# Optimization experiments

Measured on AMD Instinct MI355X. Metric: run time of the kernel, lower is better.

The kernel has to match this reference:

```python
import jax, jax.numpy as jnp
import numpy as np

D_MODEL = 1024
N_HEADS = 16
B, T = 2, 2048


def setup_inputs() -> dict:
    key = jax.random.key(0)
    ks = jax.random.split(key, 5)
    scale = 1.0 / np.sqrt(D_MODEL)
    return {
        "x": jax.random.normal(ks[0], (B, T, D_MODEL), dtype=jnp.float32),
        "W_q": jax.random.normal(ks[1], (D_MODEL, D_MODEL), dtype=jnp.float32) * scale,
        "W_k": jax.random.normal(ks[2], (D_MODEL, D_MODEL), dtype=jnp.float32) * scale,
        "W_v": jax.random.normal(ks[3], (D_MODEL, D_MODEL), dtype=jnp.float32) * scale,
        "W_o": jax.random.normal(ks[4], (D_MODEL, D_MODEL), dtype=jnp.float32) * scale,
    }


def reference(x, W_q, W_k, W_v, W_o):
    Bn, Tn, D = x.shape
    H = N_HEADS
    Dh = D // H
    # nn.Linear(x) = x @ W.T ; weights stored as [out, in]
    q = (x @ W_q.T).reshape(Bn, Tn, H, Dh).transpose(0, 2, 1, 3)  # [B,H,T,Dh]
    k = (x @ W_k.T).reshape(Bn, Tn, H, Dh).transpose(0, 2, 1, 3)
    v = (x @ W_v.T).reshape(Bn, Tn, H, Dh).transpose(0, 2, 1, 3)
    scores = jnp.einsum("bhqd,bhkd->bhqk", q, k) / np.sqrt(Dh).astype(np.float32)
    attn = jax.nn.softmax(scores, axis=-1)  # [B,H,T,T]
    out = jnp.einsum("bhqk,bhkd->bhqd", attn, v)  # [B,H,T,Dh]
    out = out.transpose(0, 2, 1, 3).reshape(Bn, Tn, D)
    return out @ W_o.T
```

## Files before the change

### kernel.cpp

```cpp
#include <hip/hip_runtime.h>
#include <stdint.h>
#include <stddef.h>


typedef __bf16  bf16x8  __attribute__((ext_vector_type(8)));
typedef __bf16  bf16x4  __attribute__((ext_vector_type(4)));
typedef float   floatx4 __attribute__((ext_vector_type(4)));
typedef short   short4v __attribute__((ext_vector_type(4)));

#define DEV static __device__ __forceinline__

DEV void ld_g2l16(const void* g, void* l) {
    __builtin_amdgcn_global_load_lds(
        (__attribute__((address_space(1))) void*)g,
        (__attribute__((address_space(3))) void*)l,
        16, 0, 0);
}

DEV floatx4 mfma16(bf16x4 a, bf16x4 b, floatx4 c) {
#if defined(__HIP_DEVICE_COMPILE__)
    return __builtin_amdgcn_mfma_f32_16x16x16bf16_1k(
        __builtin_bit_cast(short4v, a), __builtin_bit_cast(short4v, b),
        c, 0, 0, 0);
#else
    (void)a; (void)b;
    return c;
#endif
}

#define WK_SCALE 0.18033688011112042f

__global__ __launch_bounds__(256) void cvt_all(
    const float* __restrict__ x,
    const float* __restrict__ wq, const float* __restrict__ wk,
    const float* __restrict__ wv, const float* __restrict__ wo,
    __bf16* __restrict__ xb,
    __bf16* __restrict__ wqb, __bf16* __restrict__ wkb,
    __bf16* __restrict__ wvb, __bf16* __restrict__ wob)
{
    unsigned u = blockIdx.x * 256u + threadIdx.x;
    const float* src;
    __bf16* dst;
    unsigned off;
    float mul = 1.0f;
    if (u < 1048576u) {
        src = x; dst = xb; off = u;
    } else {
        unsigned u2 = u - 1048576u;
        unsigned sel = u2 >> 18;
        off = u2 & 0x3FFFFu;
        src = (sel == 0) ? wq : (sel == 1) ? wk : (sel == 2) ? wv : wo;
        dst = (sel == 0) ? wqb : (sel == 1) ? wkb : (sel == 2) ? wvb : wob;
        if (sel == 1) mul = WK_SCALE;
    }
    float4 f = *(const float4*)(src + (size_t)off * 4);
    bf16x4 o = { (__bf16)(f.x * mul), (__bf16)(f.y * mul),
                 (__bf16)(f.z * mul), (__bf16)(f.w * mul) };
    *(bf16x4*)(dst + (size_t)off * 4) = o;
}

template<int BM, int NMAT, bool OUT_F32, bool TR_V>
__global__ __launch_bounds__(256) void gemm_bt(
    const __bf16* __restrict__ A,
    const __bf16* __restrict__ B0, const __bf16* __restrict__ B1,
    const __bf16* __restrict__ B2,
    void* __restrict__ C0, void* __restrict__ C1, void* __restrict__ C2)
{
    constexpr int Kd = 1024;
    constexpr int N  = 1024;
    constexpr int MI = BM / 32;
    constexpr int NA = BM / 64;
    __shared__ __bf16 As[BM * 32];
    __shared__ __bf16 Bs[128 * 32];

    const int t    = threadIdx.x;
    const int wid  = __builtin_amdgcn_readfirstlane(t >> 6);
    const int lane = t & 63;
    const int quad = lane >> 4;
    const int l15  = lane & 15;

    const int bx  = blockIdx.x;
    const int mat = (NMAT > 1) ? (bx >> 3) : 0;
    const int bn  = (NMAT > 1) ? (bx & 7)  : bx;
    const int bm  = blockIdx.y;
    const __bf16* Bm = (mat == 0) ? B0 : (mat == 1) ? B1 : B2;

    const __bf16* pA[NA];
    const __bf16* pB[2];
#pragma unroll
    for (int i = 0; i < NA; ++i) {
        int c    = i * 256 + t;
        int row  = c >> 2;
        int g    = (c & 3) ^ ((row >> 1) & 3);
        pA[i] = A + (size_t)(bm * BM + row) * Kd + g * 8;
    }
#pragma unroll
    for (int i = 0; i < 2; ++i) {
        int c    = i * 256 + t;
        int row  = c >> 2;
        int g    = (c & 3) ^ ((row >> 1) & 3);
        pB[i] = Bm + (size_t)(bn * 128 + row) * Kd + g * 8;
    }

    const int wm = wid >> 1;
    const int wn = wid & 1;
    const int slotr = quad ^ ((l15 >> 1) & 3);

    floatx4 acc[MI][4];
    const floatx4 z = { 0.f, 0.f, 0.f, 0.f };
#pragma unroll
    for (int i = 0; i < MI; ++i)
#pragma unroll
        for (int j = 0; j < 4; ++j) acc[i][j] = z;

    for (int kb = 0; kb < Kd; kb += 32) {
        __syncthreads();
#pragma unroll
        for (int i = 0; i < NA; ++i)
            ld_g2l16(pA[i] + kb, (char*)As + i * 4096 + wid * 1024);
#pragma unroll
        for (int i = 0; i < 2; ++i)
            ld_g2l16(pB[i] + kb, (char*)Bs + i * 4096 + wid * 1024);
        __syncthreads();

        bf16x8 af[MI], bf[4];
#pragma unroll
        for (int i = 0; i < MI; ++i) {
            int rowA = wm * (BM / 2) + i * 16 + l15;
            af[i] = *(const bf16x8*)&As[rowA * 32 + slotr * 8];
        }
#pragma unroll
        for (int j = 0; j < 4; ++j) {
            int rowB = wn * 64 + j * 16 + l15;
            bf[j] = *(const bf16x8*)&Bs[rowB * 32 + slotr * 8];
        }
#pragma unroll
        for (int i = 0; i < MI; ++i)
#pragma unroll
            for (int j = 0; j < 4; ++j)
                acc[i][j] = __builtin_amdgcn_mfma_f32_16x16x32_bf16(
                    af[i], bf[j], acc[i][j], 0, 0, 0);
    }

    const int row0 = bm * BM + wm * (BM / 2);
    const int col0 = bn * 128 + wn * 64;

    if (TR_V && mat == 2) {
        __bf16* Vt = (__bf16*)C2;
        const int bq    = bm >> 4;
        const int tloc0 = (row0 & 2047) + quad * 4;
#pragma unroll
        for (int i = 0; i < MI; ++i)
#pragma unroll
            for (int j = 0; j < 4; ++j) {
                int col = col0 + j * 16 + l15;
                int hh  = col >> 6, dh = col & 63;
                bf16x4 v = { (__bf16)acc[i][j][0], (__bf16)acc[i][j][1],
                             (__bf16)acc[i][j][2], (__bf16)acc[i][j][3] };
                *(bf16x4*)(Vt + ((size_t)(bq * 16 + hh) * 64 + dh) * 2048
                              + tloc0 + i * 16) = v;
            }
    } else {
        void* Cv = (mat == 0) ? C0 : (mat == 1) ? C1 : C2;
#pragma unroll
        for (int i = 0; i < MI; ++i)
#pragma unroll
            for (int j = 0; j < 4; ++j)
#pragma unroll
                for (int r = 0; r < 4; ++r) {
                    int grow = row0 + i * 16 + quad * 4 + r;
                    int gcol = col0 + j * 16 + l15;
                    if (OUT_F32)
                        ((float*)Cv)[(size_t)grow * N + gcol] = acc[i][j][r];
                    else
                        ((__bf16*)Cv)[(size_t)grow * N + gcol] =
                            (__bf16)acc[i][j][r];
                }
    }
}

__global__ __launch_bounds__(256, 2) void flash_kernel(
    const __bf16* __restrict__ Q, const __bf16* __restrict__ K,
    const __bf16* __restrict__ Vt, __bf16* __restrict__ O)
{
    __shared__ __bf16 Qs[128 * 64];
    __shared__ __bf16 Ks[2][64 * 64];
    __shared__ __bf16 Vs[2][64 * 64];

    const int t    = threadIdx.x;
    const int wid  = __builtin_amdgcn_readfirstlane(t >> 6);
    const int half = wid >> 1;
    const int wsub = wid & 1;
    const int lane = t & 63;
    const int quad = lane >> 4;
    const int l15  = lane & 15;
    const int qt   = blockIdx.x;
    const int bh   = blockIdx.y;
    const int b    = bh >> 4, h = bh & 15;

#pragma unroll
    for (int i = 0; i < 4; ++i) {
        int c = i * 256 + t;
        int row = c >> 3;
        int g   = (c & 7) ^ (row & 7);
        ld_g2l16(Q + (size_t)(b * 2048 + qt * 128 + row) * 1024 + h * 64 + g * 8,
                 (char*)Qs + i * 4096 + wid * 1024);
    }

    const __bf16* pK[2];
    const __bf16* pV[2];
#pragma unroll
    for (int i = 0; i < 2; ++i) {
        int c = i * 256 + t;
        int srow = c >> 3;
        int sg   = (c & 7) ^ (srow & 7);
        pK[i] = K  + (size_t)(b * 2048 + srow) * 1024 + h * 64 + sg * 8;
        pV[i] = Vt + (size_t)(bh * 64 + srow) * 2048 + sg * 8;
    }

    __syncthreads();

    bf16x8 qf[4][2];
#pragma unroll
    for (int nb = 0; nb < 4; ++nb)
#pragma unroll
        for (int ks = 0; ks < 2; ++ks) {
            int row  = wsub * 64 + nb * 16 + l15;
            int slot = (ks * 4 + quad) ^ (row & 7);
            qf[nb][ks] = *(const bf16x8*)&Qs[row * 64 + slot * 8];
        }

    int koff[2];
#pragma unroll
    for (int ks = 0; ks < 2; ++ks)
        koff[ks] = l15 * 128 + (((ks * 4 + quad) ^ (l15 & 7)) << 4);
    int voff[4];
#pragma unroll
    for (int k16 = 0; k16 < 4; ++k16)
        voff[k16] = l15 * 128 + (((k16 * 2 + (quad >> 1)) ^ (l15 & 7)) << 4)
                  + (quad & 1) * 8;

    const floatx4 z = { 0.f, 0.f, 0.f, 0.f };
    floatx4 o[4][4];
#pragma unroll
    for (int nb = 0; nb < 4; ++nb)
#pragma unroll
        for (int nd = 0; nd < 4; ++nd) o[nb][nd] = z;
    float lsum[4] = { 0.f, 0.f, 0.f, 0.f };

    for (int it = 0; it < 16; ++it) {
        __syncthreads();
#pragma unroll
        for (int i = 0; i < 2; ++i) {
            ld_g2l16(pK[i] + (size_t)it * 65536,
                     (char*)Ks[0] + i * 4096 + wid * 1024);
            ld_g2l16(pK[i] + (size_t)(16 + it) * 65536,
                     (char*)Ks[1] + i * 4096 + wid * 1024);
            ld_g2l16(pV[i] + it * 64,
                     (char*)Vs[0] + i * 4096 + wid * 1024);
            ld_g2l16(pV[i] + (16 + it) * 64,
                     (char*)Vs[1] + i * 4096 + wid * 1024);
        }
        __syncthreads();

        const char* kbase = (const char*)Ks[half];
        const char* vbase = (const char*)Vs[half];
#pragma unroll
        for (int kt16 = 0; kt16 < 4; ++kt16) {
            floatx4 s[4] = { z, z, z, z };
#pragma unroll
            for (int ks = 0; ks < 2; ++ks) {
                bf16x8 kf = *(const bf16x8*)(kbase + kt16 * 2048 + koff[ks]);
#pragma unroll
                for (int nb = 0; nb < 4; ++nb)
                    s[nb] = __builtin_amdgcn_mfma_f32_16x16x32_bf16(
                        kf, qf[nb][ks], s[nb], 0, 0, 0);
            }
            bf16x4 pb[4];
#pragma unroll
            for (int nb = 0; nb < 4; ++nb) {
                float p0 = __builtin_amdgcn_exp2f(s[nb][0]);
                float p1 = __builtin_amdgcn_exp2f(s[nb][1]);
                float p2 = __builtin_amdgcn_exp2f(s[nb][2]);
                float p3 = __builtin_amdgcn_exp2f(s[nb][3]);
                lsum[nb] += (p0 + p1) + (p2 + p3);
                bf16x4 pw = { (__bf16)p0, (__bf16)p1, (__bf16)p2, (__bf16)p3 };
                pb[nb] = pw;
            }
#pragma unroll
            for (int nd = 0; nd < 4; ++nd) {
                bf16x4 va = *(const bf16x4*)(vbase + nd * 2048 + voff[kt16]);
#pragma unroll
                for (int nb = 0; nb < 4; ++nb)
                    o[nb][nd] = mfma16(va, pb[nb], o[nb][nd]);
            }
        }
    }

    __syncthreads();
    float* obuf = (wsub == 0) ? (float*)&Ks[0][0] : (float*)&Vs[0][0];
    float* lbuf = (float*)&Qs[0] + wsub * 256;
    if (half == 1) {
#pragma unroll
        for (int nb = 0; nb < 4; ++nb)
#pragma unroll
            for (int nd = 0; nd < 4; ++nd)
                *(floatx4*)(obuf + (nb * 4 + nd) * 256 + lane * 4) = o[nb][nd];
#pragma unroll
        for (int nb = 0; nb < 4; ++nb) lbuf[nb * 64 + lane] = lsum[nb];
    }
    __syncthreads();
    if (half == 0) {
#pragma unroll
        for (int nb = 0; nb < 4; ++nb)
#pragma unroll
            for (int nd = 0; nd < 4; ++nd)
                o[nb][nd] += *(const floatx4*)(obuf + (nb * 4 + nd) * 256
                                               + lane * 4);
#pragma unroll
        for (int nb = 0; nb < 4; ++nb) {
            lsum[nb] += lbuf[nb * 64 + lane];
            lsum[nb] += __shfl_xor(lsum[nb], 16);
            lsum[nb] += __shfl_xor(lsum[nb], 32);
        }
#pragma unroll
        for (int nb = 0; nb < 4; ++nb) {
            float inv = 1.f / lsum[nb];
            int token = qt * 128 + wsub * 64 + nb * 16 + l15;
#pragma unroll
            for (int nd = 0; nd < 4; ++nd) {
                bf16x4 ov = { (__bf16)(o[nb][nd][0] * inv),
                              (__bf16)(o[nb][nd][1] * inv),
                              (__bf16)(o[nb][nd][2] * inv),
                              (__bf16)(o[nb][nd][3] * inv) };
                *(bf16x4*)(O + (size_t)(b * 2048 + token) * 1024
                             + h * 64 + nd * 16 + quad * 4) = ov;
            }
        }
    }
}

extern "C" void kernel_launch(void* const* d_in, const int* in_sizes, int n_in,
                              void* d_out, int out_size, void* d_ws, size_t ws_size,
                              hipStream_t stream)
{
    const float* x  = (const float*)d_in[0];
    const float* wq = (const float*)d_in[1];
    const float* wk = (const float*)d_in[2];
    const float* wv = (const float*)d_in[3];
    const float* wo = (const float*)d_in[4];

    char* ws = (char*)d_ws;
    __bf16* xb  = (__bf16*)(ws + 0);
    __bf16* wqb = (__bf16*)(ws + 8388608);
    __bf16* wkb = (__bf16*)(ws + 10485760);
    __bf16* wvb = (__bf16*)(ws + 12582912);
    __bf16* wob = (__bf16*)(ws + 14680064);
    __bf16* Qb  = (__bf16*)(ws + 16777216);
    __bf16* Kb  = (__bf16*)(ws + 25165824);
    __bf16* Vtb = (__bf16*)(ws + 33554432);
    __bf16* Ob  = xb;

    cvt_all<<<8192, 256, 0, stream>>>(x, wq, wk, wv, wo, xb, wqb, wkb, wvb, wob);

    gemm_bt<128, 3, false, true><<<dim3(24, 32), 256, 0, stream>>>(
        xb, wqb, wkb, wvb, (void*)Qb, (void*)Kb, (void*)Vtb);

    flash_kernel<<<dim3(16, 32), 256, 0, stream>>>(Qb, Kb, Vtb, Ob);

    gemm_bt<64, 1, true, false><<<dim3(8, 64), 256, 0, stream>>>(
        Ob, wob, nullptr, nullptr, d_out, nullptr, nullptr);
}
```

Measured before the change: 176.8 us.

## Double-buffer K/V tiles in flash attention and raise MFMA wave priority

The K and V shared-memory tiles become double-buffered. The next iteration's global-to-LDS loads are issued before the current tile is computed, so memory latency overlaps the MFMA work, and the two barriers per iteration drop to one. Each MFMA section is also wrapped in s_setprio so matrix work is favoured over the exp/convert section of other waves. This raises LDS use per block, which may limit occupancy at two blocks per CU.

New measurement: 185.5 us. 1.05x slower.

```diff
diff --git a/kernel.cpp b/kernel.cpp
--- a/kernel.cpp
+++ b/kernel.cpp
@@ -184,8 +184,8 @@
     const __bf16* __restrict__ Vt, __bf16* __restrict__ O)
 {
     __shared__ __bf16 Qs[128 * 64];
-    __shared__ __bf16 Ks[2][64 * 64];
-    __shared__ __bf16 Vs[2][64 * 64];
+    __shared__ __bf16 Ks[2][2][64 * 64];
+    __shared__ __bf16 Vs[2][2][64 * 64];
 
     const int t    = threadIdx.x;
     const int wid  = __builtin_amdgcn_readfirstlane(t >> 6);
@@ -218,6 +218,21 @@
         pV[i] = Vt + (size_t)(bh * 64 + srow) * 2048 + sg * 8;
     }
 
+    auto stage_kv = [&](int it2, int buf) {
+#pragma unroll
+        for (int i = 0; i < 2; ++i) {
+            ld_g2l16(pK[i] + (size_t)it2 * 65536,
+                     (char*)Ks[buf][0] + i * 4096 + wid * 1024);
+            ld_g2l16(pK[i] + (size_t)(16 + it2) * 65536,
+                     (char*)Ks[buf][1] + i * 4096 + wid * 1024);
+            ld_g2l16(pV[i] + it2 * 64,
+                     (char*)Vs[buf][0] + i * 4096 + wid * 1024);
+            ld_g2l16(pV[i] + (16 + it2) * 64,
+                     (char*)Vs[buf][1] + i * 4096 + wid * 1024);
+        }
+    };
+
+    stage_kv(0, 0);
     __syncthreads();
 
     bf16x8 qf[4][2];
@@ -248,26 +263,16 @@
         for (int nd = 0; nd < 4; ++nd) o[nb][nd] = z;
     float lsum[4] = { 0.f, 0.f, 0.f, 0.f };
 
+    int cur = 0;
     for (int it = 0; it < 16; ++it) {
-        __syncthreads();
-#pragma unroll
-        for (int i = 0; i < 2; ++i) {
-            ld_g2l16(pK[i] + (size_t)it * 65536,
-                     (char*)Ks[0] + i * 4096 + wid * 1024);
-            ld_g2l16(pK[i] + (size_t)(16 + it) * 65536,
-                     (char*)Ks[1] + i * 4096 + wid * 1024);
-            ld_g2l16(pV[i] + it * 64,
-                     (char*)Vs[0] + i * 4096 + wid * 1024);
-            ld_g2l16(pV[i] + (16 + it) * 64,
-                     (char*)Vs[1] + i * 4096 + wid * 1024);
-        }
-        __syncthreads();
-
-        const char* kbase = (const char*)Ks[half];
-        const char* vbase = (const char*)Vs[half];
+        if (it < 15) stage_kv(it + 1, cur ^ 1);
+
+        const char* kbase = (const char*)Ks[cur][half];
+        const char* vbase = (const char*)Vs[cur][half];
 #pragma unroll
         for (int kt16 = 0; kt16 < 4; ++kt16) {
             floatx4 s[4] = { z, z, z, z };
+            __builtin_amdgcn_s_setprio(1);
 #pragma unroll
             for (int ks = 0; ks < 2; ++ks) {
                 bf16x8 kf = *(const bf16x8*)(kbase + kt16 * 2048 + koff[ks]);
@@ -276,6 +281,7 @@
                     s[nb] = __builtin_amdgcn_mfma_f32_16x16x32_bf16(
                         kf, qf[nb][ks], s[nb], 0, 0, 0);
             }
+            __builtin_amdgcn_s_setprio(0);
             bf16x4 pb[4];
 #pragma unroll
             for (int nb = 0; nb < 4; ++nb) {
@@ -287,6 +293,7 @@
                 bf16x4 pw = { (__bf16)p0, (__bf16)p1, (__bf16)p2, (__bf16)p3 };
                 pb[nb] = pw;
             }
+            __builtin_amdgcn_s_setprio(1);
 #pragma unroll
             for (int nd = 0; nd < 4; ++nd) {
                 bf16x4 va = *(const bf16x4*)(vbase + nd * 2048 + voff[kt16]);
@@ -294,11 +301,14 @@
                 for (int nb = 0; nb < 4; ++nb)
                     o[nb][nd] = mfma16(va, pb[nb], o[nb][nd]);
             }
-        }
-    }
-
-    __syncthreads();
-    float* obuf = (wsub == 0) ? (float*)&Ks[0][0] : (float*)&Vs[0][0];
+            __builtin_amdgcn_s_setprio(0);
+        }
+        __syncthreads();
+        cur ^= 1;
+    }
+
+    float* obuf = (wsub == 0) ? (float*)&Ks[0][0][0]
+                              : (float*)&Vs[0][0][0];
     float* lbuf = (float*)&Qs[0] + wsub * 256;
     if (half == 1) {
 #pragma unroll
```

## Split flash attention key range four ways per block with smaller query tiles

Applied to the files above, without the earlier changes.

The flash kernel now handles 64 query rows per block instead of 128. Each of the four waves processes a different quarter of the key sequence, in 32-key chunks per iteration, and a multi-stage LDS reduction merges the partial outputs and row sums at the end. The grid doubles to 1024 blocks, launch bounds allow 4 blocks per CU, and block indices are swizzled so that blocks sharing a head are spread out. The aim is more parallelism and occupancy to better fill the GPU, at the cost of more reduction passes and barriers and more K/V reloading per query row.

After: 273.7 us. +54.9%, slower.

```diff
diff --git a/kernel.cpp b/kernel.cpp
--- a/kernel.cpp
+++ b/kernel.cpp
@@ -179,44 +179,40 @@
     }
 }
 
-__global__ __launch_bounds__(256, 2) void flash_kernel(
+__global__ __launch_bounds__(256, 4) void flash_kernel(
     const __bf16* __restrict__ Q, const __bf16* __restrict__ K,
     const __bf16* __restrict__ Vt, __bf16* __restrict__ O)
 {
-    __shared__ __bf16 Qs[128 * 64];
-    __shared__ __bf16 Ks[2][64 * 64];
-    __shared__ __bf16 Vs[2][64 * 64];
+    __shared__ __bf16 Qs[64 * 64];
+    __shared__ __bf16 Ks[4][32 * 64];
+    __shared__ __bf16 Vs[4][64 * 32];
 
     const int t    = threadIdx.x;
     const int wid  = __builtin_amdgcn_readfirstlane(t >> 6);
-    const int half = wid >> 1;
-    const int wsub = wid & 1;
     const int lane = t & 63;
     const int quad = lane >> 4;
     const int l15  = lane & 15;
-    const int qt   = blockIdx.x;
-    const int bh   = blockIdx.y;
+    const int flat = blockIdx.y * 32 + blockIdx.x;
+    const int swz  = (flat & 7) * 128 + (flat >> 3);
+    const int qt   = swz & 31;
+    const int bh   = swz >> 5;
     const int b    = bh >> 4, h = bh & 15;
 
 #pragma unroll
-    for (int i = 0; i < 4; ++i) {
+    for (int i = 0; i < 2; ++i) {
         int c = i * 256 + t;
         int row = c >> 3;
         int g   = (c & 7) ^ (row & 7);
-        ld_g2l16(Q + (size_t)(b * 2048 + qt * 128 + row) * 1024 + h * 64 + g * 8,
+        ld_g2l16(Q + (size_t)(b * 2048 + qt * 64 + row) * 1024 + h * 64 + g * 8,
                  (char*)Qs + i * 4096 + wid * 1024);
     }
 
-    const __bf16* pK[2];
-    const __bf16* pV[2];
-#pragma unroll
-    for (int i = 0; i < 2; ++i) {
-        int c = i * 256 + t;
-        int srow = c >> 3;
-        int sg   = (c & 7) ^ (srow & 7);
-        pK[i] = K  + (size_t)(b * 2048 + srow) * 1024 + h * 64 + sg * 8;
-        pV[i] = Vt + (size_t)(bh * 64 + srow) * 2048 + sg * 8;
-    }
+    const int srowK = t >> 3;
+    const int sgK   = (t & 7) ^ (srowK & 7);
+    const __bf16* pK0 = K + (size_t)(b * 2048 + srowK) * 1024 + h * 64 + sgK * 8;
+    const int srowV = t >> 2;
+    const int sgV   = (t & 3) ^ (srowV & 3);
+    const __bf16* pV0 = Vt + (size_t)(bh * 64 + srowV) * 2048 + sgV * 8;
 
     __syncthreads();
 
@@ -225,7 +221,7 @@
     for (int nb = 0; nb < 4; ++nb)
 #pragma unroll
         for (int ks = 0; ks < 2; ++ks) {
-            int row  = wsub * 64 + nb * 16 + l15;
+            int row  = nb * 16 + l15;
             int slot = (ks * 4 + quad) ^ (row & 7);
             qf[nb][ks] = *(const bf16x8*)&Qs[row * 64 + slot * 8];
         }
@@ -234,11 +230,11 @@
 #pragma unroll
     for (int ks = 0; ks < 2; ++ks)
         koff[ks] = l15 * 128 + (((ks * 4 + quad) ^ (l15 & 7)) << 4);
-    int voff[4];
-#pragma unroll
-    for (int k16 = 0; k16 < 4; ++k16)
-        voff[k16] = l15 * 128 + (((k16 * 2 + (quad >> 1)) ^ (l15 & 7)) << 4)
-                  + (quad & 1) * 8;
+    int voff[2];
+#pragma unroll
+    for (int kt = 0; kt < 2; ++kt)
+        voff[kt] = l15 * 64 + (((kt * 2 + (quad >> 1)) ^ (l15 & 3)) << 4)
+                 + (quad & 1) * 8;
 
     const floatx4 z = { 0.f, 0.f, 0.f, 0.f };
     floatx4 o[4][4];
@@ -251,26 +247,23 @@
     for (int it = 0; it < 16; ++it) {
         __syncthreads();
 #pragma unroll
-        for (int i = 0; i < 2; ++i) {
-            ld_g2l16(pK[i] + (size_t)it * 65536,
-                     (char*)Ks[0] + i * 4096 + wid * 1024);
-            ld_g2l16(pK[i] + (size_t)(16 + it) * 65536,
-                     (char*)Ks[1] + i * 4096 + wid * 1024);
-            ld_g2l16(pV[i] + it * 64,
-                     (char*)Vs[0] + i * 4096 + wid * 1024);
-            ld_g2l16(pV[i] + (16 + it) * 64,
-                     (char*)Vs[1] + i * 4096 + wid * 1024);
-        }
+        for (int tq = 0; tq < 4; ++tq)
+            ld_g2l16(pK0 + ((size_t)tq * 512 + it * 32) * 1024,
+                     (char*)Ks + tq * 4096 + wid * 1024);
+#pragma unroll
+        for (int tq = 0; tq < 4; ++tq)
+            ld_g2l16(pV0 + tq * 512 + it * 32,
+                     (char*)Vs + tq * 4096 + wid * 1024);
         __syncthreads();
 
-        const char* kbase = (const char*)Ks[half];
-        const char* vbase = (const char*)Vs[half];
-#pragma unroll
-        for (int kt16 = 0; kt16 < 4; ++kt16) {
+        const char* kbase = (const char*)Ks + wid * 4096;
+        const char* vbase = (const char*)Vs + wid * 4096;
+#pragma unroll
+        for (int kt = 0; kt < 2; ++kt) {
             floatx4 s[4] = { z, z, z, z };
 #pragma unroll
             for (int ks = 0; ks < 2; ++ks) {
-                bf16x8 kf = *(const bf16x8*)(kbase + kt16 * 2048 + koff[ks]);
+                bf16x8 kf = *(const bf16x8*)(kbase + kt * 2048 + koff[ks]);
 #pragma unroll
                 for (int nb = 0; nb < 4; ++nb)
                     s[nb] = __builtin_amdgcn_mfma_f32_16x16x32_bf16(
@@ -289,7 +282,7 @@
             }
 #pragma unroll
             for (int nd = 0; nd < 4; ++nd) {
-                bf16x4 va = *(const bf16x4*)(vbase + nd * 2048 + voff[kt16]);
+                bf16x4 va = *(const bf16x4*)(vbase + nd * 1024 + voff[kt]);
 #pragma unroll
                 for (int nb = 0; nb < 4; ++nb)
                     o[nb][nd] = mfma16(va, pb[nb], o[nb][nd]);
@@ -298,35 +291,71 @@
     }
 
     __syncthreads();
-    float* obuf = (wsub == 0) ? (float*)&Ks[0][0] : (float*)&Vs[0][0];
-    float* lbuf = (float*)&Qs[0] + wsub * 256;
-    if (half == 1) {
-#pragma unroll
-        for (int nb = 0; nb < 4; ++nb)
-#pragma unroll
-            for (int nd = 0; nd < 4; ++nd)
-                *(floatx4*)(obuf + (nb * 4 + nd) * 256 + lane * 4) = o[nb][nd];
-#pragma unroll
-        for (int nb = 0; nb < 4; ++nb) lbuf[nb * 64 + lane] = lsum[nb];
+    float* kb = (float*)&Ks[0][0];
+    float* vb = (float*)&Vs[0][0];
+    float* lb = (float*)&Qs[0];
+#pragma unroll
+    for (int nb = 0; nb < 4; ++nb)
+        lb[wid * 256 + nb * 64 + lane] = lsum[nb];
+    if (wid == 1) {
+#pragma unroll
+        for (int nb = 0; nb < 4; ++nb)
+#pragma unroll
+            for (int nd = 0; nd < 4; ++nd)
+                *(floatx4*)(kb + (nb * 4 + nd) * 256 + lane * 4) = o[nb][nd];
+    }
+    if (wid == 3) {
+#pragma unroll
+        for (int nb = 0; nb < 4; ++nb)
+#pragma unroll
+            for (int nd = 0; nd < 4; ++nd)
+                *(floatx4*)(vb + (nb * 4 + nd) * 256 + lane * 4) = o[nb][nd];
     }
     __syncthreads();
-    if (half == 0) {
-#pragma unroll
-        for (int nb = 0; nb < 4; ++nb)
-#pragma unroll
-            for (int nd = 0; nd < 4; ++nd)
-                o[nb][nd] += *(const floatx4*)(obuf + (nb * 4 + nd) * 256
+    if (wid == 0) {
+#pragma unroll
+        for (int nb = 0; nb < 4; ++nb)
+#pragma unroll
+            for (int nd = 0; nd < 4; ++nd)
+                o[nb][nd] += *(const floatx4*)(kb + (nb * 4 + nd) * 256
                                                + lane * 4);
+    }
+    if (wid == 2) {
+#pragma unroll
+        for (int nb = 0; nb < 4; ++nb)
+#pragma unroll
+            for (int nd = 0; nd < 4; ++nd)
+                o[nb][nd] += *(const floatx4*)(vb + (nb * 4 + nd) * 256
+                                               + lane * 4);
+    }
+    __syncthreads();
+    if (wid == 2) {
+#pragma unroll
+        for (int nb = 0; nb < 4; ++nb)
+#pragma unroll
+            for (int nd = 0; nd < 4; ++nd)
+                *(floatx4*)(kb + (nb * 4 + nd) * 256 + lane * 4) = o[nb][nd];
+    }
+    __syncthreads();
+    if (wid == 0) {
+#pragma unroll
+        for (int nb = 0; nb < 4; ++nb)
+#pragma unroll
+            for (int nd = 0; nd < 4; ++nd)
+                o[nb][nd] += *(const floatx4*)(kb + (nb * 4 + nd) * 256
+                                               + lane * 4);
 #pragma unroll
         for (int nb = 0; nb < 4; ++nb) {
-            lsum[nb] += lbuf[nb * 64 + lane];
-            lsum[nb] += __shfl_xor(lsum[nb], 16);
-            lsum[nb] += __shfl_xor(lsum[nb], 32);
+            float s0 = lb[nb * 64 + lane]       + lb[256 + nb * 64 + lane]
+                     + lb[512 + nb * 64 + lane] + lb[768 + nb * 64 + lane];
+            s0 += __shfl_xor(s0, 16);
+            s0 += __shfl_xor(s0, 32);
+            lsum[nb] = s0;
         }
 #pragma unroll
         for (int nb = 0; nb < 4; ++nb) {
             float inv = 1.f / lsum[nb];
-            int token = qt * 128 + wsub * 64 + nb * 16 + l15;
+            int token = qt * 64 + nb * 16 + l15;
 #pragma unroll
             for (int nd = 0; nd < 4; ++nd) {
                 bf16x4 ov = { (__bf16)(o[nb][nd][0] * inv),
@@ -366,7 +395,7 @@
     gemm_bt<128, 3, false, true><<<dim3(24, 32), 256, 0, stream>>>(
         xb, wqb, wkb, wvb, (void*)Qb, (void*)Kb, (void*)Vtb);
 
-    flash_kernel<<<dim3(16, 32), 256, 0, stream>>>(Qb, Kb, Vtb, Ob);
+    flash_kernel<<<dim3(32, 32), 256, 0, stream>>>(Qb, Kb, Vtb, Ob);
 
     gemm_bt<64, 1, true, false><<<dim3(8, 64), 256, 0, stream>>>(
         Ob, wob, nullptr, nullptr, d_out, nullptr, nullptr);
```
